# Kernel optimization log

Measured on AMD Instinct MI355X. Metric: run time of the kernel, lower is better.

## Reference

```python
import jax, jax.numpy as jnp
import numpy as np

TAU = 2.0  # LIF membrane time constant (spikingjelly default)
SCALE = 0.125

@jax.custom_vjp
def heaviside(x):
    return (x >= 0).astype(x.dtype)

def _hv_fwd(x):
    return heaviside(x), x

def _hv_bwd(x, g):
    s = jax.nn.sigmoid(4.0 * x)  # sigmoid surrogate, alpha=4
    return (g * 4.0 * s * (1.0 - s),)

heaviside.defvjp(_hv_fwd, _hv_bwd)

def lif(x, v_th):
    """Multi-step LIF over leading time axis. x: [T, ...]. decay_input, hard reset to 0."""
    def step(v, xt):
        v = v + (xt - v) / TAU
        s = heaviside(v - v_th)
        return v * (1.0 - s), s
    return jax.lax.scan(step, jnp.zeros_like(x[0]), x)[1]

def conv1x1(x, w, b=None):
    # x: [T,B,C,N], w: [O,C]
    y = jnp.einsum('oc,tbcn->tbon', w, x)
    if b is not None:
        y = y + b[None, None, :, None]
    return y

def bn(x, p, eps=1e-5):
    # inference-mode BatchNorm1d over channel axis; p: [4,C] = gamma,beta,mean,var
    g, b, m, v = p[0], p[1], p[2], p[3]
    inv = g / jnp.sqrt(v + eps)
    return x * inv[None, None, :, None] + (b - m * inv)[None, None, :, None]

def setup_inputs() -> dict:
    key = jax.random.key(0)
    ks = jax.random.split(key, 10)
    T, B, C, H, W = 4, 32, 512, 16, 16
    wscale = 1.0 / np.sqrt(C)
    def bn_params(k):
        k1, k2, k3, k4 = jax.random.split(k, 4)
        gamma = 1.0 + 0.1 * jax.random.normal(k1, (C,))
        beta = 0.1 * jax.random.normal(k2, (C,))
        mean = 0.1 * jax.random.normal(k3, (C,))
        var = 1.0 + 0.1 * jax.random.uniform(k4, (C,))
        return jnp.stack([gamma, beta, mean, var])
    return {
        'x': jax.random.normal(ks[0], (T, B, C, H, W), dtype=jnp.float32),
        'res_attn': jnp.zeros((1,), dtype=jnp.float32),
        'q_w': wscale * jax.random.normal(ks[1], (C, C), dtype=jnp.float32),
        'k_w': wscale * jax.random.normal(ks[2], (C, C), dtype=jnp.float32),
        'v_w': wscale * jax.random.normal(ks[3], (C, C), dtype=jnp.float32),
        'proj_w': wscale * jax.random.normal(ks[4], (C, C), dtype=jnp.float32),
        'proj_b': 0.01 * jax.random.normal(ks[5], (C,), dtype=jnp.float32),
        'q_bn': bn_params(ks[6]),
        'k_bn': bn_params(ks[7]),
        'v_bn': bn_params(ks[8]),
        'p_bn': bn_params(ks[9]),
    }

def reference(x, res_attn, q_w, k_w, v_w, proj_w, proj_b, q_bn, k_bn, v_bn, p_bn):
    T, B, C, H, W = x.shape
    num_heads = 8
    d = C // num_heads
    N = H * W
    xf = x.reshape(T, B, C, N)

    def branch(w, p, v_th):
        return lif(bn(conv1x1(xf, w), p), v_th)

    def to_heads(t):  # [T,B,C,N] -> [T,B,h,N,d]
        return t.transpose(0, 1, 3, 2).reshape(T, B, N, num_heads, d).transpose(0, 1, 3, 2, 4)

    q = to_heads(branch(q_w, q_bn, 1.0))
    k = to_heads(branch(k_w, k_bn, 1.0))
    v = to_heads(branch(v_w, v_bn, 1.0))

    # linear (non-softmax) attention: q @ (k^T @ v) * scale
    kv = jnp.einsum('tbhnd,tbhne->tbhde', k, v)
    a = jnp.einsum('tbhnd,tbhde->tbhne', q, kv) * SCALE  # [T,B,h,N,d]

    # [T,B,h,N,d] -> transpose(3,4) -> [T,B,h,d,N] -> [T,B,C,N]
    a = jnp.swapaxes(a, 3, 4).reshape(T, B, C, N)
    a = lif(a, 0.5)  # attn_lif with v_threshold=0.5

    out = conv1x1(a, proj_w, proj_b)
    out = bn(out, p_bn).reshape(T, B, C, H, W)
    out = lif(out, 1.0)
    return out, v
```

## Files before the change

kernel.cpp:

```cpp
#include <hip/hip_runtime.h>
#include <stdint.h>

#define T_ 4
#define B_ 32
#define C_ 512
#define N_ 256
#define NH_ 8
#define NB_ (N_ / 8)
#define BITS_BYTES_ ((size_t)(T_ * B_ * C_) * NB_)

typedef float f32x2 __attribute__((ext_vector_type(2)));

__device__ __forceinline__ f32x2 pk_mul_d(f32x2 a, f32x2 b) {
  f32x2 r;
  asm("v_pk_mul_f32 %0, %1, %2" : "=v"(r) : "v"(a), "v"(b));
  return r;
}
__device__ __forceinline__ f32x2 pk_mul_x(f32x2 a, f32x2 b) {
  f32x2 r;
  asm("v_pk_mul_f32 %0, %1, %2 op_sel:[0,1] op_sel_hi:[1,0]"
      : "=v"(r) : "v"(a), "v"(b));
  return r;
}
__device__ __forceinline__ void pk_add_acc(f32x2& acc, f32x2 p) {
  asm("v_pk_add_f32 %0, %0, %1" : "+v"(acc) : "v"(p));
}
__device__ __forceinline__ void pk_fma_d(f32x2& acc, f32x2 a, f32x2 b) {
  asm("v_pk_fma_f32 %0, %1, %2, %0" : "+v"(acc) : "v"(a), "v"(b));
}
__device__ __forceinline__ void pk_fma_x(f32x2& acc, f32x2 a, f32x2 b) {
  asm("v_pk_fma_f32 %0, %1, %2, %0 op_sel:[0,1,0] op_sel_hi:[1,0,1]"
      : "+v"(acc) : "v"(a), "v"(b));
}


__global__ __launch_bounds__(256, 2) void qkv_gemm_lif(
    const float* __restrict__ x, const float* __restrict__ wq,
    const float* __restrict__ wk, const float* __restrict__ wv,
    const float* __restrict__ bnq, const float* __restrict__ bnk,
    const float* __restrict__ bnv,
    uint8_t* __restrict__ sbits, float* __restrict__ out1) {
#pragma clang fp contract(off)
  const int br = blockIdx.z;
  const int b  = blockIdx.y;
  const int ot = blockIdx.x >> 1, nt = blockIdx.x & 1;
  const float* w = (br == 0) ? wq : (br == 1) ? wk : wv;
  const float* bn = (br == 0) ? bnq : (br == 1) ? bnk : bnv;
  uint8_t* sb = sbits + (size_t)br * BITS_BYTES_;

  const int tid = threadIdx.x;
  const int tx = tid & 15, ty = tid >> 4;
  const int o0 = ot * 64, n0 = nt * 128;

  __shared__ float As[2][16][64];
  __shared__ float Bs[2][16][128];

  float inv[4], add[4];
#pragma unroll
  for (int i = 0; i < 4; ++i) {
    int o = o0 + ty * 4 + i;
    float g = bn[o], be = bn[C_ + o], mm = bn[2 * C_ + o], va = bn[3 * C_ + o];
    float iv = g / sqrtf(va + 1e-5f);
    inv[i] = iv;
    add[i] = be - mm * iv;
  }

  float vst[4][8];
#pragma unroll
  for (int i = 0; i < 4; ++i)
#pragma unroll
    for (int j = 0; j < 8; ++j) vst[i][j] = 0.f;

  const int sa_o = tid & 63, sa_kq = (tid >> 6) * 4;
  const int fr = tid >> 5, fq = (tid & 31) * 4;
  const int fr2 = (tid + 256) >> 5, fq2 = ((tid + 256) & 31) * 4;

  for (int t = 0; t < T_; ++t) {
    const float* xb = x + (size_t)(t * B_ + b) * (C_ * N_);
    f32x2 acc_d[2][4], acc_x[2][4];
#pragma unroll
    for (int ip = 0; ip < 2; ++ip)
#pragma unroll
      for (int jp = 0; jp < 4; ++jp) {
        acc_d[ip][jp] = (f32x2){0.f, 0.f};
        acc_x[ip][jp] = (f32x2){0.f, 0.f};
      }

    {
      float4 a4 = *(const float4*)(w + (size_t)(o0 + sa_o) * C_ + 0 + sa_kq);
      float4 b40 = *(const float4*)(xb + (size_t)(0 + fr) * N_ + n0 + fq);
      float4 b41 = *(const float4*)(xb + (size_t)(0 + fr2) * N_ + n0 + fq2);
      __syncthreads();
      As[0][sa_kq + 0][sa_o] = a4.x; As[0][sa_kq + 1][sa_o] = a4.y;
      As[0][sa_kq + 2][sa_o] = a4.z; As[0][sa_kq + 3][sa_o] = a4.w;
      *(float4*)(&Bs[0][fr][fq]) = b40;
      *(float4*)(&Bs[0][fr2][fq2]) = b41;
      __syncthreads();
    }

    for (int it = 0; it < 32; ++it) {
      const int cur = it & 1;
      float4 a4, b40, b41;
      if (it < 31) {
        int kc = (it + 1) * 16;
        a4  = *(const float4*)(w + (size_t)(o0 + sa_o) * C_ + kc + sa_kq);
        b40 = *(const float4*)(xb + (size_t)(kc + fr) * N_ + n0 + fq);
        b41 = *(const float4*)(xb + (size_t)(kc + fr2) * N_ + n0 + fq2);
      }
#pragma unroll
      for (int k = 0; k < 16; ++k) {
        float4 av4 = *(const float4*)(&As[cur][k][ty * 4]);
        float4 bq0 = *(const float4*)(&Bs[cur][k][tx * 4]);
        float4 bq1 = *(const float4*)(&Bs[cur][k][64 + tx * 4]);
        f32x2 a2[2] = {(f32x2){av4.x, av4.y}, (f32x2){av4.z, av4.w}};
        f32x2 b2[4] = {(f32x2){bq0.x, bq0.y}, (f32x2){bq0.z, bq0.w},
                       (f32x2){bq1.x, bq1.y}, (f32x2){bq1.z, bq1.w}};
#pragma unroll
        for (int ip = 0; ip < 2; ++ip)
#pragma unroll
          for (int jp = 0; jp < 4; ++jp) {
            f32x2 pd = pk_mul_d(a2[ip], b2[jp]);
            f32x2 px = pk_mul_x(a2[ip], b2[jp]);
            pk_add_acc(acc_d[ip][jp], pd);
            pk_add_acc(acc_x[ip][jp], px);
          }
      }
      if (it < 31) {
        const int nxt = cur ^ 1;
        As[nxt][sa_kq + 0][sa_o] = a4.x; As[nxt][sa_kq + 1][sa_o] = a4.y;
        As[nxt][sa_kq + 2][sa_o] = a4.z; As[nxt][sa_kq + 3][sa_o] = a4.w;
        *(float4*)(&Bs[nxt][fr][fq]) = b40;
        *(float4*)(&Bs[nxt][fr2][fq2]) = b41;
        __syncthreads();
      }
    }

    {
      size_t tb = (size_t)(t * B_ + b);
      unsigned nibsA = 0, nibsB = 0;
#pragma unroll
      for (int i = 0; i < 4; ++i) {
#pragma unroll
        for (int jj = 0; jj < 8; ++jj) {
          int ip = i >> 1, il = i & 1, jp = jj >> 1, jl = jj & 1;
          float a = (il == jl) ? acc_d[ip][jp][il] : acc_x[ip][jp][il];
          float y0 = a * inv[i];
          float y = y0 + add[i];
          float d = y - vst[i][jj];
          float vs = vst[i][jj] + d * 0.5f;
          unsigned sp = (vs >= 1.0f) ? 1u : 0u;
          vst[i][jj] = sp ? 0.f : vs;
          if (jj < 4) nibsA |= sp << (4 * i + jj);
          else        nibsB |= sp << (4 * i + jj - 4);
        }
      }
      unsigned oA = __shfl_xor(nibsA, 1);
      unsigned oB = __shfl_xor(nibsB, 1);
      int m = tx >> 1;
      if ((tx & 1) == 0) {
#pragma unroll
        for (int i = 0; i < 4; ++i) {
          int o = o0 + ty * 4 + i;
          unsigned byte_ = ((nibsA >> (4 * i)) & 0xF) | (((oA >> (4 * i)) & 0xF) << 4);
          sb[(tb * C_ + o) * NB_ + (n0 >> 3) + m] = (uint8_t)byte_;
        }
      } else {
#pragma unroll
        for (int i = 0; i < 4; ++i) {
          int o = o0 + ty * 4 + i;
          unsigned byte_ = ((oB >> (4 * i)) & 0xF) | (((nibsB >> (4 * i)) & 0xF) << 4);
          sb[(tb * C_ + o) * NB_ + (n0 >> 3) + 8 + m] = (uint8_t)byte_;
        }
      }
      if (br == 2) {
#pragma unroll
        for (int i = 0; i < 4; ++i) {
          int o = o0 + ty * 4 + i;
          int h = o >> 6, dd = o & 63;
          size_t base = ((tb * NH_ + h) * (size_t)N_) * 64 + dd;
#pragma unroll
          for (int jj = 0; jj < 8; ++jj) {
            int n = n0 + ((jj < 4) ? (tx * 4 + jj) : (64 + tx * 4 + jj - 4));
            unsigned sp = (jj < 4) ? ((nibsA >> (4 * i + jj)) & 1u)
                                   : ((nibsB >> (4 * i + jj - 4)) & 1u);
            out1[base + (size_t)n * 64] = sp ? 1.0f : 0.0f;
          }
        }
      }
    }
  }
}

__global__ __launch_bounds__(512, 1) void attn_lif(
    const uint8_t* __restrict__ bits, uint8_t* __restrict__ abits) {
#pragma clang fp contract(off)
  const unsigned long long* qb = (const unsigned long long*)bits;
  const unsigned long long* kb = qb + BITS_BYTES_ / 8;
  const unsigned long long* vb = kb + BITS_BYTES_ / 8;
  unsigned long long* ap = (unsigned long long*)abits;

  const int h = blockIdx.x, b = blockIdx.y;
  const int tid = threadIdx.x;
  const int lane = tid & 63, wave = tid >> 6;
  const int nw = wave & 3, eh = wave >> 2;

  __shared__ unsigned long long kbl[64][4];
  __shared__ unsigned long long vbl[64][4];
  __shared__ float kvl[64][64];

  float state[32];
#pragma unroll
  for (int e = 0; e < 32; ++e) state[e] = 0.f;

  for (int t = 0; t < T_; ++t) {
    size_t row0 = (size_t)(t * B_ + b) * C_ + h * 64;
    {
      int i = tid & 255, c = i >> 2, w = i & 3;
      if (tid < 256) kbl[c][w] = kb[(row0 + c) * 4 + w];
      else           vbl[c][w] = vb[(row0 + c) * 4 + w];
    }
    __syncthreads();
    {
      int d = tid & 63, eb = (tid >> 6) * 8;
#pragma unroll
      for (int e2 = 0; e2 < 8; ++e2) {
        int e = eb + e2;
        int s = 0;
#pragma unroll
        for (int w = 0; w < 4; ++w) s += __popcll(kbl[d][w] & vbl[e][w]);
        kvl[d][e] = (float)s;
      }
    }
    __syncthreads();
    float acc[32];
#pragma unroll
    for (int e = 0; e < 32; ++e) acc[e] = 0.f;
    for (int d = 0; d < 64; ++d) {
      unsigned long long qw = qb[(row0 + d) * 4 + nw];
      float qf = (float)(unsigned)((qw >> lane) & 1ULL);
      const float* kr = &kvl[d][eh * 32];
#pragma unroll
      for (int e = 0; e < 32; ++e) acc[e] = acc[e] + qf * kr[e];
    }
    {
#pragma unroll
      for (int e2 = 0; e2 < 32; ++e2) {
        int e = eh * 32 + e2;
        float a = acc[e2] * 0.125f;
        float d0 = a - state[e2];
        float vs = state[e2] + d0 * 0.5f;
        int sp = (vs >= 0.5f) ? 1 : 0;
        state[e2] = sp ? 0.f : vs;
        unsigned long long m = __ballot(sp);
        if (lane == 0) ap[(row0 + e) * 4 + nw] = m;
      }
    }
    __syncthreads();
  }
}

__global__ __launch_bounds__(256, 2) void proj_gemm_lif(
    const uint8_t* __restrict__ ab, const float* __restrict__ wp,
    const float* __restrict__ pb, const float* __restrict__ bnp,
    float* __restrict__ out0) {
  const int b = blockIdx.y;
  const int ot = blockIdx.x >> 1, nt = blockIdx.x & 1;
  const int tid = threadIdx.x;
  const int tx = tid & 15, ty = tid >> 4;
  const int o0 = ot * 64, n0 = nt * 128;

  __shared__ float As[2][16][64];
  __shared__ float Bs[2][16][128];

  float inv[4], add[4], bias[4];
  {
#pragma clang fp contract(off)
#pragma unroll
    for (int i = 0; i < 4; ++i) {
      int o = o0 + ty * 4 + i;
      float g = bnp[o], be = bnp[C_ + o], mm = bnp[2 * C_ + o], va = bnp[3 * C_ + o];
      float iv = g / sqrtf(va + 1e-5f);
      inv[i] = iv;
      add[i] = be - mm * iv;
      bias[i] = pb[o];
    }
  }

  float vst[4][8];
#pragma unroll
  for (int i = 0; i < 4; ++i)
#pragma unroll
    for (int j = 0; j < 8; ++j) vst[i][j] = 0.f;

  const int sa_o = tid & 63, sa_kq = (tid >> 6) * 4;
  const int br_ = tid >> 4, bq16 = tid & 15;

  for (int t = 0; t < T_; ++t) {
    f32x2 acc_d[2][4], acc_x[2][4];
#pragma unroll
    for (int ip = 0; ip < 2; ++ip)
#pragma unroll
      for (int jp = 0; jp < 4; ++jp) {
        acc_d[ip][jp] = (f32x2){0.f, 0.f};
        acc_x[ip][jp] = (f32x2){0.f, 0.f};
      }
    size_t tb = (size_t)(t * B_ + b);

    {
      float4 a4 = *(const float4*)(wp + (size_t)(o0 + sa_o) * C_ + 0 + sa_kq);
      uint8_t by = ab[(tb * C_ + 0 + br_) * NB_ + (n0 >> 3) + bq16];
      __syncthreads();
      As[0][sa_kq + 0][sa_o] = a4.x; As[0][sa_kq + 1][sa_o] = a4.y;
      As[0][sa_kq + 2][sa_o] = a4.z; As[0][sa_kq + 3][sa_o] = a4.w;
      int nb = bq16 * 8;
#pragma unroll
      for (int j = 0; j < 8; ++j) Bs[0][br_][nb + j] = (float)((by >> j) & 1);
      __syncthreads();
    }

    for (int it = 0; it < 32; ++it) {
      const int cur = it & 1;
      float4 a4; uint8_t by = 0;
      if (it < 31) {
        int kc = (it + 1) * 16;
        a4 = *(const float4*)(wp + (size_t)(o0 + sa_o) * C_ + kc + sa_kq);
        by = ab[(tb * C_ + kc + br_) * NB_ + (n0 >> 3) + bq16];
      }
#pragma unroll
      for (int k = 0; k < 16; ++k) {
        float4 av4 = *(const float4*)(&As[cur][k][ty * 4]);
        float4 bq0 = *(const float4*)(&Bs[cur][k][tx * 4]);
        float4 bq1 = *(const float4*)(&Bs[cur][k][64 + tx * 4]);
        f32x2 a2[2] = {(f32x2){av4.x, av4.y}, (f32x2){av4.z, av4.w}};
        f32x2 b2[4] = {(f32x2){bq0.x, bq0.y}, (f32x2){bq0.z, bq0.w},
                       (f32x2){bq1.x, bq1.y}, (f32x2){bq1.z, bq1.w}};
#pragma unroll
        for (int ip = 0; ip < 2; ++ip)
#pragma unroll
          for (int jp = 0; jp < 4; ++jp) {
            pk_fma_d(acc_d[ip][jp], a2[ip], b2[jp]);
            pk_fma_x(acc_x[ip][jp], a2[ip], b2[jp]);
          }
      }
      if (it < 31) {
        const int nxt = cur ^ 1;
        As[nxt][sa_kq + 0][sa_o] = a4.x; As[nxt][sa_kq + 1][sa_o] = a4.y;
        As[nxt][sa_kq + 2][sa_o] = a4.z; As[nxt][sa_kq + 3][sa_o] = a4.w;
        int nb = bq16 * 8;
#pragma unroll
        for (int j = 0; j < 8; ++j) Bs[nxt][br_][nb + j] = (float)((by >> j) & 1);
        __syncthreads();
      }
    }

    {
#pragma clang fp contract(off)
#pragma unroll
      for (int i = 0; i < 4; ++i) {
        int o = o0 + ty * 4 + i;
        float4 r0, r1;
#pragma unroll
        for (int jj = 0; jj < 8; ++jj) {
          int ip = i >> 1, il = i & 1, jp = jj >> 1, jl = jj & 1;
          float a = (il == jl) ? acc_d[ip][jp][il] : acc_x[ip][jp][il];
          float y1 = a + bias[i];
          float y2 = y1 * inv[i];
          float y = y2 + add[i];
          float d0 = y - vst[i][jj];
          float vs = vst[i][jj] + d0 * 0.5f;
          int sp = (vs >= 1.0f) ? 1 : 0;
          vst[i][jj] = sp ? 0.f : vs;
          if (jj < 4) (&r0.x)[jj] = sp ? 1.0f : 0.0f;
          else        (&r1.x)[jj - 4] = sp ? 1.0f : 0.0f;
        }
        float* dst = out0 + (tb * C_ + o) * N_ + n0;
        *(float4*)(dst + tx * 4) = r0;
        *(float4*)(dst + 64 + tx * 4) = r1;
      }
    }
  }
}


extern "C" void kernel_launch(void* const* d_in, const int* in_sizes, int n_in,
                              void* d_out, int out_size, void* d_ws, size_t ws_size,
                              hipStream_t stream) {
  const float* x   = (const float*)d_in[0];
  const float* qw  = (const float*)d_in[2];
  const float* kw  = (const float*)d_in[3];
  const float* vw  = (const float*)d_in[4];
  const float* pw  = (const float*)d_in[5];
  const float* pbb = (const float*)d_in[6];
  const float* qbn = (const float*)d_in[7];
  const float* kbn = (const float*)d_in[8];
  const float* vbn = (const float*)d_in[9];
  const float* pbn = (const float*)d_in[10];

  uint8_t* bits  = (uint8_t*)d_ws;
  uint8_t* abits = bits + 3 * BITS_BYTES_;

  float* out0 = (float*)d_out;
  float* out1 = out0 + (size_t)T_ * B_ * C_ * N_;

  qkv_gemm_lif<<<dim3(16, 32, 3), dim3(256), 0, stream>>>(
      x, qw, kw, vw, qbn, kbn, vbn, bits, out1);
  attn_lif<<<dim3(8, 32), dim3(512), 0, stream>>>(bits, abits);
  proj_gemm_lif<<<dim3(16, 32), dim3(256), 0, stream>>>(abits, pw, pbb, pbn,
                                                        out0);
}
```

Baseline: 1.275 ms.

## Shrink QKV GEMM tile to 32x128 with 128 threads and drop smem double buffering

The QKV GEMM+LIF kernel goes from 256 threads with 64x128 output tiles to 128 threads with 32x128 tiles, which doubles the grid along the output-channel axis. Launch bounds change to allow 4 blocks per CU. The double-buffered shared-memory pipeline is replaced by a single-buffered loop that loads, syncs, then computes. This cuts LDS use and is meant to raise occupancy, but it gives up the overlap of global loads with compute and halves A-tile reuse of each loaded x tile.

```diff
diff --git a/kernel.cpp b/kernel.cpp
--- a/kernel.cpp
+++ b/kernel.cpp
@@ -34,7 +34,7 @@
 }
 
 
-__global__ __launch_bounds__(256, 2) void qkv_gemm_lif(
+__global__ __launch_bounds__(128, 4) void qkv_gemm_lif(
     const float* __restrict__ x, const float* __restrict__ wq,
     const float* __restrict__ wk, const float* __restrict__ wv,
     const float* __restrict__ bnq, const float* __restrict__ bnk,
@@ -50,10 +50,10 @@
 
   const int tid = threadIdx.x;
   const int tx = tid & 15, ty = tid >> 4;
-  const int o0 = ot * 64, n0 = nt * 128;
-
-  __shared__ float As[2][16][64];
-  __shared__ float Bs[2][16][128];
+  const int o0 = ot * 32, n0 = nt * 128;
+
+  __shared__ float As[16][32];
+  __shared__ float Bs[16][128];
 
   float inv[4], add[4];
 #pragma unroll
@@ -71,9 +71,7 @@
 #pragma unroll
     for (int j = 0; j < 8; ++j) vst[i][j] = 0.f;
 
-  const int sa_o = tid & 63, sa_kq = (tid >> 6) * 4;
-  const int fr = tid >> 5, fq = (tid & 31) * 4;
-  const int fr2 = (tid + 256) >> 5, fq2 = ((tid + 256) & 31) * 4;
+  const int sa_o = tid & 31, sa_kq = (tid >> 5) * 4;
 
   for (int t = 0; t < T_; ++t) {
     const float* xb = x + (size_t)(t * B_ + b) * (C_ * N_);
@@ -86,32 +84,30 @@
         acc_x[ip][jp] = (f32x2){0.f, 0.f};
       }
 
-    {
-      float4 a4 = *(const float4*)(w + (size_t)(o0 + sa_o) * C_ + 0 + sa_kq);
-      float4 b40 = *(const float4*)(xb + (size_t)(0 + fr) * N_ + n0 + fq);
-      float4 b41 = *(const float4*)(xb + (size_t)(0 + fr2) * N_ + n0 + fq2);
+    for (int kc = 0; kc < C_; kc += 16) {
+      float4 a4 = *(const float4*)(w + (size_t)(o0 + sa_o) * C_ + kc + sa_kq);
+      float4 bb[4];
+#pragma unroll
+      for (int r = 0; r < 4; ++r) {
+        int slot = tid + r * 128;
+        int fr = slot >> 5, fq = (slot & 31) * 4;
+        bb[r] = *(const float4*)(xb + (size_t)(kc + fr) * N_ + n0 + fq);
+      }
       __syncthreads();
-      As[0][sa_kq + 0][sa_o] = a4.x; As[0][sa_kq + 1][sa_o] = a4.y;
-      As[0][sa_kq + 2][sa_o] = a4.z; As[0][sa_kq + 3][sa_o] = a4.w;
-      *(float4*)(&Bs[0][fr][fq]) = b40;
-      *(float4*)(&Bs[0][fr2][fq2]) = b41;
+      As[sa_kq + 0][sa_o] = a4.x; As[sa_kq + 1][sa_o] = a4.y;
+      As[sa_kq + 2][sa_o] = a4.z; As[sa_kq + 3][sa_o] = a4.w;
+#pragma unroll
+      for (int r = 0; r < 4; ++r) {
+        int slot = tid + r * 128;
+        int fr = slot >> 5, fq = (slot & 31) * 4;
+        *(float4*)(&Bs[fr][fq]) = bb[r];
+      }
       __syncthreads();
-    }
-
-    for (int it = 0; it < 32; ++it) {
-      const int cur = it & 1;
-      float4 a4, b40, b41;
-      if (it < 31) {
-        int kc = (it + 1) * 16;
-        a4  = *(const float4*)(w + (size_t)(o0 + sa_o) * C_ + kc + sa_kq);
-        b40 = *(const float4*)(xb + (size_t)(kc + fr) * N_ + n0 + fq);
-        b41 = *(const float4*)(xb + (size_t)(kc + fr2) * N_ + n0 + fq2);
-      }
 #pragma unroll
       for (int k = 0; k < 16; ++k) {
-        float4 av4 = *(const float4*)(&As[cur][k][ty * 4]);
-        float4 bq0 = *(const float4*)(&Bs[cur][k][tx * 4]);
-        float4 bq1 = *(const float4*)(&Bs[cur][k][64 + tx * 4]);
+        float4 av4 = *(const float4*)(&As[k][ty * 4]);
+        float4 bq0 = *(const float4*)(&Bs[k][tx * 4]);
+        float4 bq1 = *(const float4*)(&Bs[k][64 + tx * 4]);
         f32x2 a2[2] = {(f32x2){av4.x, av4.y}, (f32x2){av4.z, av4.w}};
         f32x2 b2[4] = {(f32x2){bq0.x, bq0.y}, (f32x2){bq0.z, bq0.w},
                        (f32x2){bq1.x, bq1.y}, (f32x2){bq1.z, bq1.w}};
@@ -125,15 +121,8 @@
             pk_add_acc(acc_x[ip][jp], px);
           }
       }
-      if (it < 31) {
-        const int nxt = cur ^ 1;
-        As[nxt][sa_kq + 0][sa_o] = a4.x; As[nxt][sa_kq + 1][sa_o] = a4.y;
-        As[nxt][sa_kq + 2][sa_o] = a4.z; As[nxt][sa_kq + 3][sa_o] = a4.w;
-        *(float4*)(&Bs[nxt][fr][fq]) = b40;
-        *(float4*)(&Bs[nxt][fr2][fq2]) = b41;
-        __syncthreads();
-      }
-    }
+    }
+    __syncthreads();
 
     {
       size_t tb = (size_t)(t * B_ + b);
@@ -402,7 +391,7 @@
   float* out0 = (float*)d_out;
   float* out1 = out0 + (size_t)T_ * B_ * C_ * N_;
 
-  qkv_gemm_lif<<<dim3(16, 32, 3), dim3(256), 0, stream>>>(
+  qkv_gemm_lif<<<dim3(32, 32, 3), dim3(128), 0, stream>>>(
       x, qw, kw, vw, qbn, kbn, vbn, bits, out1);
   attn_lif<<<dim3(8, 32), dim3(512), 0, stream>>>(bits, abits);
   proj_gemm_lif<<<dim3(16, 32), dim3(256), 0, stream>>>(abits, pw, pbb, pbn,
```

New measurement: 1.733 ms. +35.9%, slower.
